# Performance work log

Hardware: AMD Instinct MI355X
Metric: run time of the kernel (lower is better)

The kernel has to match this reference:

```python
import jax, jax.numpy as jnp
import numpy as np

HEADS = 6


def setup_inputs() -> dict:
    key = jax.random.key(0)
    ks = jax.random.split(key, 4)
    B, N, C = 4, 1024, 384
    s = 0.02
    return {
        "x": jax.random.normal(ks[0], (B, N, C), jnp.float32),
        "qkv_w": jax.random.normal(ks[1], (C, 3 * C), jnp.float32) * s,  # (in, out) layout
        "qkv_b": jnp.zeros((3 * C,), jnp.float32),
        "proj_w": jax.random.normal(ks[2], (C, C), jnp.float32) * s,
        "proj_b": jnp.zeros((C,), jnp.float32),
        "conv_w": jax.random.normal(ks[3], (HEADS, HEADS), jnp.float32) * s,  # 1x1 conv kernel (out_ch, in_ch)
        "conv_b": jnp.zeros((HEADS,), jnp.float32),
    }


def _forward(x, qkv_w, qkv_b, proj_w, proj_b, conv_w, conv_b):
    B, N, C = x.shape
    H = HEADS
    D = C // H
    scale = D ** -0.5
    qkv = (x @ qkv_w + qkv_b).reshape(B, N, 3, H, D)
    q = jnp.transpose(qkv[:, :, 0], (0, 2, 1, 3))  # bhnd
    k = jnp.transpose(qkv[:, :, 1], (0, 2, 1, 3))
    v = jnp.transpose(qkv[:, :, 2], (0, 2, 1, 3))
    qk = jnp.einsum('bhnd,bhmd->bhnm', q, k)          # raw scores (pre-scale)
    attn_mean = jax.nn.softmax(qk * scale, axis=-1)
    # data_uncertainty: 1x1 conv mixing the head channels of qk
    u = jnp.einsum('oh,bhnm->bonm', conv_w, qk) + conv_b[None, :, None, None]
    # norm_uncertainty: log(exp(u)) == u (kept faithful), then (tanh+1)/2
    u = jnp.log(jnp.exp(u))
    u = (jnp.tanh(u) + 1.0) * 0.5
    # gumbel-softmax (hard, tau=1) over logits [u, 1-u]; channel 1 selected.
    # softmax over 2 classes == sigmoid of logit difference; hard == argmax.
    gk = jax.random.key(42)
    g0 = jax.random.gumbel(jax.random.fold_in(gk, 0), u.shape, u.dtype)
    g1 = jax.random.gumbel(jax.random.fold_in(gk, 1), u.shape, u.dtype)
    l0 = u + g0
    l1 = (1.0 - u) + g1
    soft1 = jax.nn.sigmoid(l1 - l0)
    hard1 = (l1 > l0).astype(u.dtype)
    mask = hard1 + soft1 - jax.lax.stop_gradient(soft1)  # straight-through estimator
    attn = attn_mean * mask  # attn_drop is identity in eval / dropout=0
    out = jnp.einsum('bhnm,bhmd->bnhd', attn, v).reshape(B, N, C)
    out = out @ proj_w + proj_b  # proj_drop identity
    return out, attn_mean, u


def reference(x, qkv_w, qkv_b, proj_w, proj_b, conv_w, conv_b):
    return _forward(x, qkv_w, qkv_b, proj_w, proj_b, conv_w, conv_b)
```

## Files before the change

kernel.cpp:

```cpp
#include <hip/hip_runtime.h>
#include <hip/hip_bf16.h>
#include <stdint.h>
#include <stddef.h>

#define B_ 4
#define N_ 1024
#define C_ 384
#define H_ 6
#define D_ 64
#define TC_ 1152
#define BHNN_ 25165824
#define SCALE 0.125f
#define LOG2E 1.4426950408889634f
#define LN2 0.6931471805599453f

typedef __hip_bfloat16 bf16;
typedef __attribute__((ext_vector_type(4))) float f32x4;
typedef __attribute__((ext_vector_type(8))) short short8;

__device__ __forceinline__ short f2bs(float x){
  bf16 b = __float2bfloat16(x);
  return *reinterpret_cast<short*>(&b);
}

#define TFR(x0,x1,r) { x0 += x1; x1 = ((x1)<<(r))|((x1)>>(32-(r))); x1 ^= x0; }

__host__ __device__ __forceinline__ void tf2x32(uint32_t k0, uint32_t k1,
                                                uint32_t& x0, uint32_t& x1){
  uint32_t k2 = k0 ^ k1 ^ 0x1BD11BDAu;
  x0 += k0; x1 += k1;
  TFR(x0,x1,13) TFR(x0,x1,15) TFR(x0,x1,26) TFR(x0,x1,6)
  x0 += k1; x1 += k2 + 1u;
  TFR(x0,x1,17) TFR(x0,x1,29) TFR(x0,x1,16) TFR(x0,x1,24)
  x0 += k2; x1 += k0 + 2u;
  TFR(x0,x1,13) TFR(x0,x1,15) TFR(x0,x1,26) TFR(x0,x1,6)
  x0 += k0; x1 += k1 + 3u;
  TFR(x0,x1,17) TFR(x0,x1,29) TFR(x0,x1,16) TFR(x0,x1,24)
  x0 += k1; x1 += k2 + 4u;
  TFR(x0,x1,13) TFR(x0,x1,15) TFR(x0,x1,26) TFR(x0,x1,6)
  x0 += k2; x1 += k0 + 5u;
}

__device__ __forceinline__ uint32_t rotl32(uint32_t x, uint32_t r){
#if __has_builtin(__builtin_amdgcn_alignbit)
  return __builtin_amdgcn_alignbit(x, x, 32u - r);
#else
  return (x << r) | (x >> (32u - r));
#endif
}

__device__ __forceinline__ void tf_dual(uint32_t j,
    uint32_t ak0, uint32_t ak1, uint32_t ak2,
    uint32_t bk0, uint32_t bk1, uint32_t bk2,
    float& fA, float& fB){
  uint32_t x0 = ak0, x1 = j + ak1;
  uint32_t y0 = bk0, y1 = j + bk1;
  #define DTFR(r) { x0 += x1; y0 += y1;               \
                    x1 = rotl32(x1,(r)); y1 = rotl32(y1,(r)); \
                    x1 ^= x0; y1 ^= y0; }
  DTFR(13) DTFR(15) DTFR(26) DTFR(6)
  x0 += ak1; x1 += ak2 + 1u;  y0 += bk1; y1 += bk2 + 1u;
  DTFR(17) DTFR(29) DTFR(16) DTFR(24)
  x0 += ak2; x1 += ak0 + 2u;  y0 += bk2; y1 += bk0 + 2u;
  DTFR(13) DTFR(15) DTFR(26) DTFR(6)
  x0 += ak0; x1 += ak1 + 3u;  y0 += bk0; y1 += bk1 + 3u;
  DTFR(17) DTFR(29) DTFR(16) DTFR(24)
  x0 += ak1; x1 += ak2 + 4u;  y0 += bk1; y1 += bk2 + 4u;
  DTFR(13) DTFR(15) DTFR(26) DTFR(6)
  x0 += ak2; x1 += ak0 + 5u;  y0 += bk2; y1 += bk0 + 5u;
  #undef DTFR
  uint32_t bitsA = x0 ^ x1;
  uint32_t bitsB = y0 ^ y1;
  fA = fmaxf(__uint_as_float((bitsA >> 9) | 0x3F800000u) - 1.0f, 1.1754943508222875e-38f);
  fB = fmaxf(__uint_as_float((bitsB >> 9) | 0x3F800000u) - 1.0f, 1.1754943508222875e-38f);
}

__global__ __launch_bounds__(256) void k_qkv(const float* __restrict__ x,
                                             const float* __restrict__ w,
                                             const float* __restrict__ bias,
                                             bf16* __restrict__ qb,
                                             bf16* __restrict__ kb,
                                             bf16* __restrict__ vTb){
  __shared__ float As[16][68];
  __shared__ float Bs[16][68];
  const int t  = threadIdx.x;
  const int tx = t & 15, ty = t >> 4;
  const int m0 = blockIdx.x * 64, n0 = blockIdx.y * 64;
  float c[4][4] = {};
  for (int k0 = 0; k0 < C_; k0 += 16){
    #pragma unroll
    for (int i = 0; i < 4; i++){
      int idx = t + 256*i;
      int m = idx >> 4, k = idx & 15;
      As[k][m] = x[(size_t)(m0+m)*C_ + k0 + k];
      int n = idx & 63, k2 = idx >> 6;
      Bs[k2][n] = w[(size_t)(k0+k2)*TC_ + n0 + n];
    }
    __syncthreads();
    #pragma unroll
    for (int k = 0; k < 16; k++){
      float av[4], bv[4];
      #pragma unroll
      for (int i = 0; i < 4; i++) av[i] = As[k][ty*4+i];
      #pragma unroll
      for (int j = 0; j < 4; j++) bv[j] = Bs[k][tx*4+j];
      #pragma unroll
      for (int i = 0; i < 4; i++)
        #pragma unroll
        for (int j = 0; j < 4; j++) c[i][j] += av[i]*bv[j];
    }
    __syncthreads();
  }
  #pragma unroll
  for (int i = 0; i < 4; i++){
    int mg = m0 + ty*4 + i;
    int bb = mg >> 10, nn = mg & 1023;
    #pragma unroll
    for (int j = 0; j < 4; j++){
      int jg = n0 + tx*4 + j;
      int t3 = jg / C_;
      int rem = jg - t3*C_;
      int h = rem >> 6, d = rem & 63;
      bf16 val = __float2bfloat16(c[i][j] + bias[jg]);
      if (t3 == 0)      qb[((size_t)(bb*H_ + h)*N_ + nn)*D_ + d] = val;
      else if (t3 == 1) kb[((size_t)(bb*H_ + h)*N_ + nn)*D_ + d] = val;
      else              vTb[((size_t)(bb*H_ + h)*D_ + d)*N_ + nn] = val;
    }
  }
}

__global__ __launch_bounds__(256) void k_scores(const short* __restrict__ qb,
                                                const short* __restrict__ kb,
                                                float* __restrict__ qk){
  const int gw = blockIdx.x * 4 + (threadIdx.x >> 6);
  const int lane = threadIdx.x & 63;
  const int mt = gw & 63, nt = (gw >> 6) & 63, bh = gw >> 12;
  const int lo = lane & 15, quad = lane >> 4;
  const short* qrow = qb + ((size_t)bh*N_ + nt*16 + lo)*D_ + quad*8;
  const short* krow = kb + ((size_t)bh*N_ + mt*16 + lo)*D_ + quad*8;
  short8 a0 = *(const short8*)qrow;
  short8 b0 = *(const short8*)krow;
  short8 a1 = *(const short8*)(qrow + 32);
  short8 b1 = *(const short8*)(krow + 32);
  f32x4 acc = {0.f, 0.f, 0.f, 0.f};
  acc = __builtin_amdgcn_mfma_f32_16x16x32_bf16(a0, b0, acc, 0, 0, 0);
  acc = __builtin_amdgcn_mfma_f32_16x16x32_bf16(a1, b1, acc, 0, 0, 0);
  float* o = qk + (size_t)bh*N_*N_ + (size_t)(nt*16)*N_ + mt*16;
  #pragma unroll
  for (int r = 0; r < 4; r++)
    o[(size_t)(quad*4 + r)*N_ + lo] = acc[r];
}

__global__ __launch_bounds__(256) void k_fuse(float* __restrict__ attn,
                                              const float* __restrict__ cw,
                                              const float* __restrict__ cb,
                                              float* __restrict__ u_out,
                                              unsigned long long* __restrict__ mbits,
                                              uint32_t g0k0, uint32_t g0k1,
                                              uint32_t g1k0, uint32_t g1k1){
  const int bn = blockIdx.x;
  const int bb = bn >> 10, n = bn & 1023;
  const int t = threadIdx.x, lane = t & 63, wid = t >> 6;
  __shared__ float redm[H_][4], reds[H_][4];

  float qv[H_][4];
  #pragma unroll
  for (int h = 0; h < H_; h++){
    const float* p = attn + (((size_t)(bb*H_ + h) << 10) + n) * N_;
    #pragma unroll
    for (int i = 0; i < 4; i++) qv[h][i] = p[t + 256*i];
  }
  #pragma unroll
  for (int h = 0; h < H_; h++){
    float mx = fmaxf(fmaxf(qv[h][0], qv[h][1]), fmaxf(qv[h][2], qv[h][3]));
    #pragma unroll
    for (int off = 32; off > 0; off >>= 1) mx = fmaxf(mx, __shfl_xor(mx, off));
    if (lane == 0) redm[h][wid] = mx;
  }
  __syncthreads();
  float mxh[H_], sm[H_];
  #pragma unroll
  for (int h = 0; h < H_; h++){
    mxh[h] = fmaxf(fmaxf(redm[h][0], redm[h][1]), fmaxf(redm[h][2], redm[h][3]));
    const float k2 = SCALE * LOG2E;
    float s = 0.f;
    #pragma unroll
    for (int i = 0; i < 4; i++) s += __builtin_amdgcn_exp2f((qv[h][i] - mxh[h]) * k2);
    #pragma unroll
    for (int off = 32; off > 0; off >>= 1) s += __shfl_xor(s, off);
    if (lane == 0) reds[h][wid] = s;
    sm[h] = s;
  }
  __syncthreads();
  float invS[H_];
  #pragma unroll
  for (int h = 0; h < H_; h++){
    float S = reds[h][0] + reds[h][1] + reds[h][2] + reds[h][3];
    invS[h] = __builtin_amdgcn_rcpf(S);
  }
  #pragma unroll
  for (int h = 0; h < H_; h++){
    float* p = attn + (((size_t)(bb*H_ + h) << 10) + n) * N_;
    const float k2 = SCALE * LOG2E;
    #pragma unroll
    for (int i = 0; i < 4; i++)
      p[t + 256*i] = __builtin_amdgcn_exp2f((qv[h][i] - mxh[h]) * k2) * invS[h];
  }
  const uint32_t a2 = g0k0 ^ g0k1 ^ 0x1BD11BDAu;
  const uint32_t b2 = g1k0 ^ g1k1 ^ 0x1BD11BDAu;
  const uint32_t jrow = ((uint32_t)(bb*H_) << 20) | ((uint32_t)n << 10);
  #pragma unroll
  for (int i = 0; i < 4; i++){
    const uint32_t m = (uint32_t)(t + 256*i);
    #pragma unroll
    for (int o = 0; o < H_; o++){
      float up = cb[o];
      #pragma unroll
      for (int h = 0; h < H_; h++) up += cw[o*H_ + h] * qv[h][i];
      float eneg = __builtin_amdgcn_exp2f(-2.0f * LOG2E * up);
      float uu   = __builtin_amdgcn_rcpf(1.0f + eneg);
      float tt   = 2.0f * uu - 1.0f;
      float et   = __builtin_amdgcn_exp2f(tt * LOG2E);
      uint32_t j = jrow + ((uint32_t)o << 20) + m;
      float f0, f1;
      tf_dual(j, g0k0, g0k1, a2, g1k0, g1k1, b2, f0, f1);
      float L0 = __builtin_amdgcn_logf(f0);
      float L1 = __builtin_amdgcn_logf(f1);
      int hard = L0 < L1 * et;
      u_out[(size_t)j] = uu;
      unsigned long long bal = __ballot(hard);
      if (lane == 0) mbits[(size_t)j >> 6] = bal;
    }
  }
}

__global__ __launch_bounds__(256) void k_av(const float* __restrict__ attn,
                                            const unsigned long long* __restrict__ mbits,
                                            const short* __restrict__ vTb,
                                            float* __restrict__ tmp){
  const int gw = blockIdx.x * 4 + (threadIdx.x >> 6);
  const int lane = threadIdx.x & 63;
  const int pr = gw & 1, nt = (gw >> 1) & 63, bh = gw >> 7;
  const int bb = bh / H_, h = bh - bb*H_;
  const int lo = lane & 15, quad = lane >> 4;
  const int row = nt*16 + lo;
  const float* arow = attn + ((size_t)bh*N_ + row)*N_ + quad*8;
  const unsigned long long* mrow = mbits + (((size_t)bh*N_ + row)*N_ >> 6);
  const short* vrow0 = vTb + ((size_t)bh*D_ + pr*32 + lo)*N_ + quad*8;
  const short* vrow1 = vrow0 + 16*N_;
  f32x4 acc0 = {0.f, 0.f, 0.f, 0.f};
  f32x4 acc1 = {0.f, 0.f, 0.f, 0.f};
  for (int m0 = 0; m0 < N_; m0 += 32){
    f32x4 av0 = *(const f32x4*)(arow + m0);
    f32x4 av1 = *(const f32x4*)(arow + m0 + 4);
    unsigned long long wb = mrow[(m0 + quad*8) >> 6];
    int base = (m0 + quad*8) & 63;
    float vals[8] = {av0[0], av0[1], av0[2], av0[3], av1[0], av1[1], av1[2], av1[3]};
    short8 a;
    #pragma unroll
    for (int j = 0; j < 8; j++)
      a[j] = f2bs(((wb >> (base + j)) & 1ull) ? vals[j] : 0.0f);
    short8 b0 = *(const short8*)(vrow0 + m0);
    short8 b1 = *(const short8*)(vrow1 + m0);
    acc0 = __builtin_amdgcn_mfma_f32_16x16x32_bf16(a, b0, acc0, 0, 0, 0);
    acc1 = __builtin_amdgcn_mfma_f32_16x16x32_bf16(a, b1, acc1, 0, 0, 0);
  }
  float* o = tmp + ((size_t)(bb*N_) + nt*16)*C_ + h*D_ + pr*32;
  #pragma unroll
  for (int r = 0; r < 4; r++){
    o[(size_t)(quad*4 + r)*C_ + lo]      = acc0[r];
    o[(size_t)(quad*4 + r)*C_ + 16 + lo] = acc1[r];
  }
}

__global__ __launch_bounds__(256) void k_proj(const float* __restrict__ A,
                                              const float* __restrict__ w,
                                              const float* __restrict__ bias,
                                              float* __restrict__ out){
  __shared__ float As[16][36];
  __shared__ float Bs[16][68];
  const int t = threadIdx.x, tx = t & 15, ty = t >> 4;
  const int m0 = blockIdx.x * 32, n0 = blockIdx.y * 64;
  float c[2][4] = {};
  for (int k0 = 0; k0 < C_; k0 += 16){
    {
      int idx = t;
      int m = idx >> 4, k = idx & 15;
      As[k][m] = A[(size_t)(m0+m)*C_ + k0 + k];
      idx = t + 256;
      m = idx >> 4; k = idx & 15;
      As[k][m] = A[(size_t)(m0+m)*C_ + k0 + k];
    }
    #pragma unroll
    for (int i = 0; i < 4; i++){
      int idx = t + 256*i;
      int n = idx & 63, k2 = idx >> 6;
      Bs[k2][n] = w[(size_t)(k0+k2)*C_ + n0 + n];
    }
    __syncthreads();
    #pragma unroll
    for (int k = 0; k < 16; k++){
      float av[2], bv[4];
      #pragma unroll
      for (int i = 0; i < 2; i++) av[i] = As[k][ty*2+i];
      #pragma unroll
      for (int j = 0; j < 4; j++) bv[j] = Bs[k][tx*4+j];
      #pragma unroll
      for (int i = 0; i < 2; i++)
        #pragma unroll
        for (int j = 0; j < 4; j++) c[i][j] += av[i]*bv[j];
    }
    __syncthreads();
  }
  #pragma unroll
  for (int i = 0; i < 2; i++)
    #pragma unroll
    for (int j = 0; j < 4; j++)
      out[(size_t)(m0+ty*2+i)*C_ + n0+tx*4+j] = c[i][j] + bias[n0+tx*4+j];
}

extern "C" void kernel_launch(void* const* d_in, const int* in_sizes, int n_in,
                              void* d_out, int out_size, void* d_ws, size_t ws_size,
                              hipStream_t stream) {
  const float* x      = (const float*)d_in[0];
  const float* qkv_w  = (const float*)d_in[1];
  const float* qkv_b  = (const float*)d_in[2];
  const float* proj_w = (const float*)d_in[3];
  const float* proj_b = (const float*)d_in[4];
  const float* conv_w = (const float*)d_in[5];
  const float* conv_b = (const float*)d_in[6];

  float* out      = (float*)d_out;
  float* attn_out = out + (size_t)B_*N_*C_;
  float* u_out    = attn_out + (size_t)BHNN_;

  char* ws = (char*)d_ws;
  bf16* qb   = (bf16*)ws;
  bf16* kb   = (bf16*)(ws + 3145728);
  bf16* vTb  = (bf16*)(ws + 6291456);
  unsigned long long* mbits = (unsigned long long*)(ws + 9437184);
  float* tmp = (float*)(ws + 12582912);

  uint32_t g0k0, g0k1, g1k0, g1k1;
  { uint32_t a = 0u, b = 0u; tf2x32(0u, 42u, a, b); g0k0 = a; g0k1 = b; }
  { uint32_t a = 0u, b = 1u; tf2x32(0u, 42u, a, b); g1k0 = a; g1k1 = b; }

  dim3 blk(256);
  k_qkv   <<<dim3(64, 18),  blk, 0, stream>>>(x, qkv_w, qkv_b, qb, kb, vTb);
  k_scores<<<dim3(24576),   blk, 0, stream>>>((const short*)qb, (const short*)kb, attn_out);
  k_fuse  <<<dim3(4096),    blk, 0, stream>>>(attn_out, conv_w, conv_b,
                                              u_out, mbits,
                                              g0k0, g0k1, g1k0, g1k1);
  k_av    <<<dim3(768),     blk, 0, stream>>>(attn_out, mbits, (const short*)vTb, tmp);
  k_proj  <<<dim3(128, 6),  blk, 0, stream>>>(tmp, proj_w, proj_b, out);
}
```

Before: 481.4 us.

## Use packed FMA and vector loads in GEMMs; reuse softmax exponentials

```diff
diff --git a/kernel.cpp b/kernel.cpp
--- a/kernel.cpp
+++ b/kernel.cpp
@@ -15,12 +15,22 @@
 #define LN2 0.6931471805599453f
 
 typedef __hip_bfloat16 bf16;
+typedef __attribute__((ext_vector_type(2))) float f32x2;
 typedef __attribute__((ext_vector_type(4))) float f32x4;
 typedef __attribute__((ext_vector_type(8))) short short8;
+
+union f4u { f32x4 v4; f32x2 v2[2]; };
 
 __device__ __forceinline__ short f2bs(float x){
   bf16 b = __float2bfloat16(x);
   return *reinterpret_cast<short*>(&b);
+}
+
+__device__ __forceinline__ void pk_fma_ll(f32x2& c, f32x2 a, f32x2 b){
+  asm("v_pk_fma_f32 %0, %1, %2, %0 op_sel:[0,0,0] op_sel_hi:[0,1,1]" : "+v"(c) : "v"(a), "v"(b));
+}
+__device__ __forceinline__ void pk_fma_hh(f32x2& c, f32x2 a, f32x2 b){
+  asm("v_pk_fma_f32 %0, %1, %2, %0 op_sel:[1,0,0] op_sel_hi:[1,1,1]" : "+v"(c) : "v"(a), "v"(b));
 }
 
 #define TFR(x0,x1,r) { x0 += x1; x1 = ((x1)<<(r))|((x1)>>(32-(r))); x1 ^= x0; }
@@ -81,50 +91,50 @@
                                              bf16* __restrict__ qb,
                                              bf16* __restrict__ kb,
                                              bf16* __restrict__ vTb){
-  __shared__ float As[16][68];
-  __shared__ float Bs[16][68];
+  __shared__ __align__(16) float As[16][68];
+  __shared__ __align__(16) float Bs[16][68];
   const int t  = threadIdx.x;
   const int tx = t & 15, ty = t >> 4;
   const int m0 = blockIdx.x * 64, n0 = blockIdx.y * 64;
-  float c[4][4] = {};
+  const int am = t >> 2,        ak = (t & 3) * 4;
+  const int bn = (t & 15) * 4,  bk = t >> 4;
+  f32x2 c[4][2] = {};
   for (int k0 = 0; k0 < C_; k0 += 16){
-    #pragma unroll
-    for (int i = 0; i < 4; i++){
-      int idx = t + 256*i;
-      int m = idx >> 4, k = idx & 15;
-      As[k][m] = x[(size_t)(m0+m)*C_ + k0 + k];
-      int n = idx & 63, k2 = idx >> 6;
-      Bs[k2][n] = w[(size_t)(k0+k2)*TC_ + n0 + n];
-    }
+    f32x4 av = *(const f32x4*)&x[(size_t)(m0+am)*C_ + k0 + ak];
+    f32x4 bv = *(const f32x4*)&w[(size_t)(k0+bk)*TC_ + n0 + bn];
     __syncthreads();
+    As[ak+0][am] = av[0]; As[ak+1][am] = av[1];
+    As[ak+2][am] = av[2]; As[ak+3][am] = av[3];
+    *(f32x4*)&Bs[bk][bn] = bv;
+    __syncthreads();
     #pragma unroll
     for (int k = 0; k < 16; k++){
-      float av[4], bv[4];
-      #pragma unroll
-      for (int i = 0; i < 4; i++) av[i] = As[k][ty*4+i];
-      #pragma unroll
-      for (int j = 0; j < 4; j++) bv[j] = Bs[k][tx*4+j];
-      #pragma unroll
-      for (int i = 0; i < 4; i++)
-        #pragma unroll
-        for (int j = 0; j < 4; j++) c[i][j] += av[i]*bv[j];
-    }
-    __syncthreads();
+      f4u a, b;
+      a.v4 = *(const f32x4*)&As[k][ty*4];
+      b.v4 = *(const f32x4*)&Bs[k][tx*4];
+      pk_fma_ll(c[0][0], a.v2[0], b.v2[0]); pk_fma_ll(c[0][1], a.v2[0], b.v2[1]);
+      pk_fma_hh(c[1][0], a.v2[0], b.v2[0]); pk_fma_hh(c[1][1], a.v2[0], b.v2[1]);
+      pk_fma_ll(c[2][0], a.v2[1], b.v2[0]); pk_fma_ll(c[2][1], a.v2[1], b.v2[1]);
+      pk_fma_hh(c[3][0], a.v2[1], b.v2[0]); pk_fma_hh(c[3][1], a.v2[1], b.v2[1]);
+    }
   }
   #pragma unroll
   for (int i = 0; i < 4; i++){
     int mg = m0 + ty*4 + i;
     int bb = mg >> 10, nn = mg & 1023;
     #pragma unroll
-    for (int j = 0; j < 4; j++){
-      int jg = n0 + tx*4 + j;
-      int t3 = jg / C_;
-      int rem = jg - t3*C_;
-      int h = rem >> 6, d = rem & 63;
-      bf16 val = __float2bfloat16(c[i][j] + bias[jg]);
-      if (t3 == 0)      qb[((size_t)(bb*H_ + h)*N_ + nn)*D_ + d] = val;
-      else if (t3 == 1) kb[((size_t)(bb*H_ + h)*N_ + nn)*D_ + d] = val;
-      else              vTb[((size_t)(bb*H_ + h)*D_ + d)*N_ + nn] = val;
+    for (int jp = 0; jp < 2; jp++){
+      #pragma unroll
+      for (int sub = 0; sub < 2; sub++){
+        int jg = n0 + tx*4 + jp*2 + sub;
+        int t3 = jg / C_;
+        int rem = jg - t3*C_;
+        int h = rem >> 6, d = rem & 63;
+        bf16 val = __float2bfloat16(c[i][jp][sub] + bias[jg]);
+        if (t3 == 0)      qb[((size_t)(bb*H_ + h)*N_ + nn)*D_ + d] = val;
+        else if (t3 == 1) kb[((size_t)(bb*H_ + h)*N_ + nn)*D_ + d] = val;
+        else              vTb[((size_t)(bb*H_ + h)*D_ + d)*N_ + nn] = val;
+      }
     }
   }
 }
@@ -178,18 +188,37 @@
     if (lane == 0) redm[h][wid] = mx;
   }
   __syncthreads();
-  float mxh[H_], sm[H_];
+  float up[H_][4];
+  #pragma unroll
+  for (int o = 0; o < H_; o++){
+    float cbo = cb[o];
+    #pragma unroll
+    for (int i = 0; i < 4; i++) up[o][i] = cbo;
+  }
+  #pragma unroll
+  for (int h = 0; h < H_; h++){
+    #pragma unroll
+    for (int o = 0; o < H_; o++){
+      float wv = cw[o*H_ + h];
+      #pragma unroll
+      for (int i = 0; i < 4; i++) up[o][i] = fmaf(wv, qv[h][i], up[o][i]);
+    }
+  }
+  float mxh[H_];
   #pragma unroll
   for (int h = 0; h < H_; h++){
     mxh[h] = fmaxf(fmaxf(redm[h][0], redm[h][1]), fmaxf(redm[h][2], redm[h][3]));
     const float k2 = SCALE * LOG2E;
     float s = 0.f;
     #pragma unroll
-    for (int i = 0; i < 4; i++) s += __builtin_amdgcn_exp2f((qv[h][i] - mxh[h]) * k2);
+    for (int i = 0; i < 4; i++){
+      float e = __builtin_amdgcn_exp2f((qv[h][i] - mxh[h]) * k2);
+      qv[h][i] = e;
+      s += e;
+    }
     #pragma unroll
     for (int off = 32; off > 0; off >>= 1) s += __shfl_xor(s, off);
     if (lane == 0) reds[h][wid] = s;
-    sm[h] = s;
   }
   __syncthreads();
   float invS[H_];
@@ -201,35 +230,34 @@
   #pragma unroll
   for (int h = 0; h < H_; h++){
     float* p = attn + (((size_t)(bb*H_ + h) << 10) + n) * N_;
-    const float k2 = SCALE * LOG2E;
     #pragma unroll
     for (int i = 0; i < 4; i++)
-      p[t + 256*i] = __builtin_amdgcn_exp2f((qv[h][i] - mxh[h]) * k2) * invS[h];
-  }
-  const uint32_t a2 = g0k0 ^ g0k1 ^ 0x1BD11BDAu;
-  const uint32_t b2 = g1k0 ^ g1k1 ^ 0x1BD11BDAu;
+      p[t + 256*i] = qv[h][i] * invS[h];
+  }
+  const uint32_t a2k = g0k0 ^ g0k1 ^ 0x1BD11BDAu;
+  const uint32_t b2k = g1k0 ^ g1k1 ^ 0x1BD11BDAu;
   const uint32_t jrow = ((uint32_t)(bb*H_) << 20) | ((uint32_t)n << 10);
   #pragma unroll
-  for (int i = 0; i < 4; i++){
-    const uint32_t m = (uint32_t)(t + 256*i);
-    #pragma unroll
-    for (int o = 0; o < H_; o++){
-      float up = cb[o];
-      #pragma unroll
-      for (int h = 0; h < H_; h++) up += cw[o*H_ + h] * qv[h][i];
-      float eneg = __builtin_amdgcn_exp2f(-2.0f * LOG2E * up);
+  for (int o = 0; o < H_; o++){
+    float* uop = u_out + jrow + ((uint32_t)o << 20);
+    unsigned long long* mbp = mbits + ((jrow + ((uint32_t)o << 20)) >> 6);
+    #pragma unroll
+    for (int i = 0; i < 4; i++){
+      const uint32_t m = (uint32_t)(t + 256*i);
+      float upv = up[o][i];
+      float eneg = __builtin_amdgcn_exp2f(-2.0f * LOG2E * upv);
       float uu   = __builtin_amdgcn_rcpf(1.0f + eneg);
       float tt   = 2.0f * uu - 1.0f;
       float et   = __builtin_amdgcn_exp2f(tt * LOG2E);
       uint32_t j = jrow + ((uint32_t)o << 20) + m;
       float f0, f1;
-      tf_dual(j, g0k0, g0k1, a2, g1k0, g1k1, b2, f0, f1);
+      tf_dual(j, g0k0, g0k1, a2k, g1k0, g1k1, b2k, f0, f1);
       float L0 = __builtin_amdgcn_logf(f0);
       float L1 = __builtin_amdgcn_logf(f1);
       int hard = L0 < L1 * et;
-      u_out[(size_t)j] = uu;
+      uop[m] = uu;
       unsigned long long bal = __ballot(hard);
-      if (lane == 0) mbits[(size_t)j >> 6] = bal;
+      if (lane == 0) mbp[m >> 6] = bal;
     }
   }
 }
@@ -277,46 +305,37 @@
                                               const float* __restrict__ w,
                                               const float* __restrict__ bias,
                                               float* __restrict__ out){
-  __shared__ float As[16][36];
-  __shared__ float Bs[16][68];
+  __shared__ __align__(16) float As[16][36];
+  __shared__ __align__(16) float Bs[16][68];
   const int t = threadIdx.x, tx = t & 15, ty = t >> 4;
   const int m0 = blockIdx.x * 32, n0 = blockIdx.y * 64;
-  float c[2][4] = {};
+  const int am = t >> 3,        ak = (t & 7) * 2;
+  const int bn = (t & 15) * 4,  bk = t >> 4;
+  f32x2 c[2][2] = {};
   for (int k0 = 0; k0 < C_; k0 += 16){
-    {
-      int idx = t;
-      int m = idx >> 4, k = idx & 15;
-      As[k][m] = A[(size_t)(m0+m)*C_ + k0 + k];
-      idx = t + 256;
-      m = idx >> 4; k = idx & 15;
-      As[k][m] = A[(size_t)(m0+m)*C_ + k0 + k];
-    }
-    #pragma unroll
-    for (int i = 0; i < 4; i++){
-      int idx = t + 256*i;
-      int n = idx & 63, k2 = idx >> 6;
-      Bs[k2][n] = w[(size_t)(k0+k2)*C_ + n0 + n];
-    }
+    f32x2 av = *(const f32x2*)&A[(size_t)(m0+am)*C_ + k0 + ak];
+    f32x4 bv = *(const f32x4*)&w[(size_t)(k0+bk)*C_ + n0 + bn];
     __syncthreads();
+    As[ak+0][am] = av[0]; As[ak+1][am] = av[1];
+    *(f32x4*)&Bs[bk][bn] = bv;
+    __syncthreads();
     #pragma unroll
     for (int k = 0; k < 16; k++){
-      float av[2], bv[4];
+      f32x2 a2 = *(const f32x2*)&As[k][ty*2];
+      f4u b; b.v4 = *(const f32x4*)&Bs[k][tx*4];
+      pk_fma_ll(c[0][0], a2, b.v2[0]); pk_fma_ll(c[0][1], a2, b.v2[1]);
+      pk_fma_hh(c[1][0], a2, b.v2[0]); pk_fma_hh(c[1][1], a2, b.v2[1]);
+    }
+  }
+  #pragma unroll
+  for (int i = 0; i < 2; i++)
+    #pragma unroll
+    for (int jp = 0; jp < 2; jp++)
       #pragma unroll
-      for (int i = 0; i < 2; i++) av[i] = As[k][ty*2+i];
-      #pragma unroll
-      for (int j = 0; j < 4; j++) bv[j] = Bs[k][tx*4+j];
-      #pragma unroll
-      for (int i = 0; i < 2; i++)
-        #pragma unroll
-        for (int j = 0; j < 4; j++) c[i][j] += av[i]*bv[j];
-    }
-    __syncthreads();
-  }
-  #pragma unroll
-  for (int i = 0; i < 2; i++)
-    #pragma unroll
-    for (int j = 0; j < 4; j++)
-      out[(size_t)(m0+ty*2+i)*C_ + n0+tx*4+j] = c[i][j] + bias[n0+tx*4+j];
+      for (int sub = 0; sub < 2; sub++){
+        int jg = n0 + tx*4 + jp*2 + sub;
+        out[(size_t)(m0+ty*2+i)*C_ + jg] = c[i][jp][sub] + bias[jg];
+      }
 }
 
 extern "C" void kernel_launch(void* const* d_in, const int* in_sizes, int n_in,
```

After: 466.3 us. -3.1%, faster.
